# Performance work log

Hardware: AMD Instinct MI355X
Metric: run time of the kernel (lower is better)

Reference implementation:

```python
import jax, jax.numpy as jnp
import numpy as np

N, E, F_IN, H, L, G, NH, HD, C = 50000, 640000, 64, 128, 3, 64, 8, 16, 2


def setup_inputs() -> dict:
    key = jax.random.key(0)
    k = jax.random.split(key, 12)
    s = 0.02
    return {
        "x": jax.random.normal(k[0], (N, F_IN), jnp.float32),
        "edge_index": jax.random.randint(k[1], (2, E), 0, N),
        "batch_idx": jnp.sort(jax.random.randint(k[2], (N,), 0, G)),
        "emb_w": jax.random.normal(k[3], (H, F_IN), jnp.float32) * s,
        "emb_b": jnp.zeros((H,), jnp.float32),
        "gcn_w": jax.random.normal(k[4], (L, H, H), jnp.float32) * s,
        "gcn_b": jnp.zeros((L, H), jnp.float32),
        "lstm_w_ih": jax.random.normal(k[5], (4 * H, H), jnp.float32) * s,
        "lstm_w_hh": jax.random.normal(k[6], (4 * H, H), jnp.float32) * s,
        "lstm_b_ih": jnp.zeros((4 * H,), jnp.float32),
        "lstm_b_hh": jnp.zeros((4 * H,), jnp.float32),
        "attn_in_w": jax.random.normal(k[7], (3 * H, H), jnp.float32) * s,
        "attn_in_b": jnp.zeros((3 * H,), jnp.float32),
        "attn_out_w": jax.random.normal(k[8], (H, H), jnp.float32) * s,
        "attn_out_b": jnp.zeros((H,), jnp.float32),
        "cls_w1": jax.random.normal(k[9], (H // 2, H), jnp.float32) * s,
        "cls_b1": jnp.zeros((H // 2,), jnp.float32),
        "cls_w2": jax.random.normal(k[10], (C, H // 2), jnp.float32) * s,
        "cls_b2": jnp.zeros((C,), jnp.float32),
    }


def reference(x, edge_index, batch_idx, emb_w, emb_b, gcn_w, gcn_b,
              lstm_w_ih, lstm_w_hh, lstm_b_ih, lstm_b_hh,
              attn_in_w, attn_in_b, attn_out_w, attn_out_b,
              cls_w1, cls_b1, cls_w2, cls_b2):
    src, dst = edge_index[0], edge_index[1]
    # GCN symmetric norm with self-loops (PyG gcn_norm): deg includes the self loop
    deg = jax.ops.segment_sum(jnp.ones((E,), x.dtype), dst, num_segments=N) + 1.0
    dis = jax.lax.rsqrt(deg)                      # deg^{-1/2}, deg >= 1
    norm = dis[src] * dis[dst]                    # [E]
    self_norm = dis * dis                         # [N], self-loop weight

    h = x @ emb_w.T + emb_b                       # node embedding [N, H]
    for l in range(L):
        hw = h @ gcn_w[l].T                       # linear transform [N, H]
        agg = jax.ops.segment_sum(hw[src] * norm[:, None], dst, num_segments=N)
        agg = agg + hw * self_norm[:, None]       # self-loop contribution
        h = jax.nn.relu(agg + gcn_b[l])

    # global mean pool per graph
    sums = jax.ops.segment_sum(h, batch_idx, num_segments=G)
    counts = jax.ops.segment_sum(jnp.ones((N,), h.dtype), batch_idx, num_segments=G)
    ge = sums / jnp.maximum(counts, 1.0)[:, None]  # [G, H]

    # LSTM with seq_len=1, h0=c0=0 (W_hh term vanishes); gate order i,f,g,o
    gates = ge @ lstm_w_ih.T + lstm_b_ih + lstm_b_hh
    i, f, g, o = jnp.split(gates, 4, axis=-1)
    c = jax.nn.sigmoid(i) * jnp.tanh(g)
    hs = jax.nn.sigmoid(o) * jnp.tanh(c)           # [G, H]

    # MultiheadAttention, seq_len=1 self-attention
    q, kk, v = jnp.split(hs @ attn_in_w.T + attn_in_b, 3, axis=-1)
    qh = q.reshape(G, NH, HD)
    kh = kk.reshape(G, NH, HD)
    vh = v.reshape(G, NH, HD)
    scores = jnp.einsum('bhd,bhd->bh', qh, kh) / jnp.sqrt(jnp.asarray(HD, hs.dtype))
    attn = jax.nn.softmax(scores[..., None], axis=-1)[..., 0]  # single key -> all ones
    ctx = (attn[..., None] * vh).reshape(G, H)
    fe = ctx @ attn_out_w.T + attn_out_b           # attended_out.mean(dim=1) with S=1

    # classifier (dropout is identity at inference)
    z = jax.nn.relu(fe @ cls_w1.T + cls_b1)
    return z @ cls_w2.T + cls_b2
```

## Files before the change

kernel.cpp:

```cpp
#include <hip/hip_runtime.h>
#include <math.h>

#define N_NODES 50000
#define N_EDGES 640000
#define F_INDIM 64
#define HDIM 128
#define NLAYERS 3
#define NGRAPH 64
#define NCLS 2
#define SCAN_BLOCKS ((N_NODES + 255) / 256)
#define POOL_SPLIT 8
#define NTILES (N_NODES / 16)

typedef __attribute__((ext_vector_type(8))) short bf16x8;
typedef __attribute__((ext_vector_type(4))) float f32x4;

__device__ __forceinline__ float bf_lo(unsigned v) { return __uint_as_float(v << 16); }
__device__ __forceinline__ float bf_hi(unsigned v) { return __uint_as_float(v & 0xffff0000u); }
__device__ __forceinline__ unsigned short f2bf(float f) {
    unsigned b = __float_as_uint(f);
    return (unsigned short)((b + 0x7fffu + ((b >> 16) & 1u)) >> 16);
}


__global__ __launch_bounds__(256) void k_init(int* cnt, float* pool, float* counts) {
    int i = blockIdx.x * 256 + threadIdx.x;
    if (i < N_NODES) cnt[i] = 0;
    if (i < NGRAPH * HDIM) pool[i] = 0.f;
    if (i < NGRAPH) counts[i] = 0.f;
}

__global__ __launch_bounds__(256) void k_rank(const int* __restrict__ dst,
                                              int* __restrict__ cnt,
                                              int* __restrict__ rank) {
    int e = blockIdx.x * 256 + threadIdx.x;
    if (e < N_EDGES) rank[e] = atomicAdd(&cnt[dst[e]], 1);
}

__global__ __launch_bounds__(256) void k_scan1(const int* __restrict__ hist,
                                               int* __restrict__ row_start,
                                               int* __restrict__ partials,
                                               float* __restrict__ dis) {
    __shared__ int buf[256];
    int i = blockIdx.x * 256 + threadIdx.x;
    int v = (i < N_NODES) ? hist[i] : 0;
    if (i < N_NODES) dis[i] = rsqrtf((float)v + 1.0f);
    buf[threadIdx.x] = v;
    __syncthreads();
#pragma unroll
    for (int off = 1; off < 256; off <<= 1) {
        int t = (threadIdx.x >= off) ? buf[threadIdx.x - off] : 0;
        __syncthreads();
        buf[threadIdx.x] += t;
        __syncthreads();
    }
    if (i < N_NODES) row_start[i] = buf[threadIdx.x] - v;
    if (threadIdx.x == 255) partials[blockIdx.x] = buf[255];
}

__global__ __launch_bounds__(256) void k_scan2(int* __restrict__ partials) {
    __shared__ int buf[256];
    int v = (threadIdx.x < SCAN_BLOCKS) ? partials[threadIdx.x] : 0;
    buf[threadIdx.x] = v;
    __syncthreads();
#pragma unroll
    for (int off = 1; off < 256; off <<= 1) {
        int t = (threadIdx.x >= off) ? buf[threadIdx.x - off] : 0;
        __syncthreads();
        buf[threadIdx.x] += t;
        __syncthreads();
    }
    if (threadIdx.x < SCAN_BLOCKS) partials[threadIdx.x] = buf[threadIdx.x] - v;
}

__global__ __launch_bounds__(256) void k_scan3(int* __restrict__ row_start,
                                               const int* __restrict__ partials) {
    int i = blockIdx.x * 256 + threadIdx.x;
    if (i < N_NODES) row_start[i] += partials[blockIdx.x];
    if (i == 0) row_start[N_NODES] = N_EDGES;
}

__global__ __launch_bounds__(256) void k_place(const int* __restrict__ src,
                                               const int* __restrict__ dst,
                                               const int* __restrict__ rank,
                                               const float* __restrict__ dis,
                                               const int* __restrict__ row_start,
                                               uint2* __restrict__ csr) {
    int e = blockIdx.x * 256 + threadIdx.x;
    if (e >= N_EDGES) return;
    int s = src[e], d = dst[e];
    uint2 rec;
    rec.x = (unsigned)s;
    rec.y = __float_as_uint(dis[s] * dis[d]);
    csr[row_start[d] + rank[e]] = rec;
}

#define CVT_Q1 (N_NODES * F_INDIM / 4)
#define CVT_Q2 (CVT_Q1 + HDIM * F_INDIM / 4)
#define CVT_Q3 (CVT_Q2 + NLAYERS * HDIM * HDIM / 4)

__global__ __launch_bounds__(256) void k_cvt_all(const float* __restrict__ x,
                                                 const float* __restrict__ emb_w,
                                                 const float* __restrict__ gcn_w,
                                                 unsigned short* __restrict__ dst0) {
    int i = blockIdx.x * 256 + threadIdx.x;
    if (i >= CVT_Q3) return;
    const float* s;
    int off;
    if (i < CVT_Q1)      { s = x;     off = i; }
    else if (i < CVT_Q2) { s = emb_w; off = i - CVT_Q1; }
    else                 { s = gcn_w; off = i - CVT_Q2; }
    float4 v = *(const float4*)&s[off * 4];
    unsigned r0 = (unsigned)f2bf(v.x) | ((unsigned)f2bf(v.y) << 16);
    unsigned r1 = (unsigned)f2bf(v.z) | ((unsigned)f2bf(v.w) << 16);
    *(uint2*)&dst0[i * 4] = make_uint2(r0, r1);
}


template<int K>
__global__ __launch_bounds__(256) void k_mm(const unsigned short* __restrict__ A,
                                            const unsigned short* __restrict__ W,
                                            const float* __restrict__ bias,
                                            unsigned short* __restrict__ C) {
    constexpr int KS = K / 32;
    int lane = threadIdx.x & 63;
    int lg = lane >> 4, lr = lane & 15;
    int cb = (threadIdx.x >> 6) * 32;
    int tile0 = blockIdx.x * 4;

    bf16x8 wf[2][KS];
#pragma unroll
    for (int ct = 0; ct < 2; ++ct)
#pragma unroll
        for (int ks = 0; ks < KS; ++ks)
            wf[ct][ks] = *(const bf16x8*)&W[(size_t)(cb + ct * 16 + lr) * K + ks * 32 + lg * 8];

    float b0 = bias ? bias[cb + lr] : 0.f;
    float b1 = bias ? bias[cb + 16 + lr] : 0.f;

    int ntile = NTILES - tile0; if (ntile > 4) ntile = 4;
    for (int t = 0; t < ntile; ++t) {
        int rb = (tile0 + t) * 16;
        f32x4 acc0 = {0.f, 0.f, 0.f, 0.f}, acc1 = {0.f, 0.f, 0.f, 0.f};
#pragma unroll
        for (int ks = 0; ks < KS; ++ks) {
            bf16x8 af = *(const bf16x8*)&A[(size_t)(rb + lr) * K + ks * 32 + lg * 8];
            acc0 = __builtin_amdgcn_mfma_f32_16x16x32_bf16(af, wf[0][ks], acc0, 0, 0, 0);
            acc1 = __builtin_amdgcn_mfma_f32_16x16x32_bf16(af, wf[1][ks], acc1, 0, 0, 0);
        }
        int row = rb + lg * 4;
#pragma unroll
        for (int j = 0; j < 4; ++j) {
            C[(size_t)(row + j) * HDIM + cb + lr]      = f2bf(acc0[j] + b0);
            C[(size_t)(row + j) * HDIM + cb + 16 + lr] = f2bf(acc1[j] + b1);
        }
    }
}


__global__ __launch_bounds__(256) void k_gather(const unsigned short* __restrict__ hw,
                                                const int* __restrict__ row_start,
                                                const uint2* __restrict__ csr,
                                                const float* __restrict__ dis,
                                                const float* __restrict__ bias,
                                                unsigned short* __restrict__ hout) {
    int n = blockIdx.x * 4 + (threadIdx.x >> 6);
    int lane = threadIdx.x & 63;
    int half = lane >> 5;
    int cl = lane & 31;
    int beg = row_start[n], end = row_start[n + 1];
    float a0 = 0.f, a1 = 0.f, a2 = 0.f, a3 = 0.f;
    for (int e = beg; e < end; e += 16) {
        unsigned sidx[8]; float w[8]; uint2 v[8];
#pragma unroll
        for (int u = 0; u < 8; ++u) {
            int me = e + 2 * u + half;
            uint2 rec = csr[min(me, end - 1)];
            sidx[u] = rec.x;
            w[u] = (me < end) ? __uint_as_float(rec.y) : 0.f;
        }
#pragma unroll
        for (int u = 0; u < 8; ++u)
            v[u] = *(const uint2*)&hw[(size_t)sidx[u] * HDIM + cl * 4];
#pragma unroll
        for (int u = 0; u < 8; ++u) {
            a0 += w[u] * bf_lo(v[u].x);
            a1 += w[u] * bf_hi(v[u].x);
            a2 += w[u] * bf_lo(v[u].y);
            a3 += w[u] * bf_hi(v[u].y);
        }
    }
    a0 += __shfl_xor(a0, 32); a1 += __shfl_xor(a1, 32);
    a2 += __shfl_xor(a2, 32); a3 += __shfl_xor(a3, 32);
    if (half == 0) {
        float dn = dis[n], sn = dn * dn;
        uint2 vs = *(const uint2*)&hw[(size_t)n * HDIM + cl * 4];
        a0 += sn * bf_lo(vs.x); a1 += sn * bf_hi(vs.x);
        a2 += sn * bf_lo(vs.y); a3 += sn * bf_hi(vs.y);
        float4 b = *(const float4*)&bias[cl * 4];
        a0 = fmaxf(a0 + b.x, 0.f); a1 = fmaxf(a1 + b.y, 0.f);
        a2 = fmaxf(a2 + b.z, 0.f); a3 = fmaxf(a3 + b.w, 0.f);
        uint2 r;
        r.x = (unsigned)f2bf(a0) | ((unsigned)f2bf(a1) << 16);
        r.y = (unsigned)f2bf(a2) | ((unsigned)f2bf(a3) << 16);
        *(uint2*)&hout[(size_t)n * HDIM + cl * 4] = r;
    }
}


__global__ __launch_bounds__(256) void k_pool(const unsigned short* __restrict__ h,
                                              const int* __restrict__ batch,
                                              float* __restrict__ pool,
                                              float* __restrict__ counts) {
    int g  = blockIdx.x >> 3;
    int sp = blockIdx.x & 7;
    int s, e;
    {
        int lo = 0, hi = N_NODES;
        while (lo < hi) { int mid = (lo + hi) >> 1; if (batch[mid] < g) lo = mid + 1; else hi = mid; }
        s = lo;
        lo = s; hi = N_NODES;
        while (lo < hi) { int mid = (lo + hi) >> 1; if (batch[mid] < g + 1) lo = mid + 1; else hi = mid; }
        e = lo;
    }
    int len = e - s;
    int chunk = (len + POOL_SPLIT - 1) / POOL_SPLIT;
    int ss = s + sp * chunk;
    int ee = min(ss + chunk, e);
    int cp = threadIdx.x & 63;
    int r  = threadIdx.x >> 6;
    float a0 = 0.f, a1 = 0.f;
    for (int n = ss + r; n < ee; n += 4) {
        unsigned v = *(const unsigned*)&h[(size_t)n * HDIM + cp * 2];
        a0 += bf_lo(v);
        a1 += bf_hi(v);
    }
    __shared__ float red0[4][64], red1[4][64];
    red0[r][cp] = a0; red1[r][cp] = a1;
    __syncthreads();
    if (r == 0) {
#pragma unroll
        for (int j = 1; j < 4; ++j) { a0 += red0[j][cp]; a1 += red1[j][cp]; }
        atomicAdd(&pool[g * HDIM + cp * 2], a0);
        atomicAdd(&pool[g * HDIM + cp * 2 + 1], a1);
    }
    if (threadIdx.x == 0 && ee > ss) atomicAdd(&counts[g], (float)(ee - ss));
}


__global__ __launch_bounds__(128) void k_tail(const float* __restrict__ pool,
                                              const float* __restrict__ counts,
                                              const float* __restrict__ w_ih,
                                              const float* __restrict__ b_ih,
                                              const float* __restrict__ b_hh,
                                              const float* __restrict__ attn_in_w,
                                              const float* __restrict__ attn_in_b,
                                              const float* __restrict__ attn_out_w,
                                              const float* __restrict__ attn_out_b,
                                              const float* __restrict__ w1,
                                              const float* __restrict__ b1,
                                              const float* __restrict__ w2,
                                              const float* __restrict__ b2,
                                              float* __restrict__ out) {
    __shared__ float ge[128], hsr[128], vv[128], fe[128], zz[64];
    int g = blockIdx.x, t = threadIdx.x;
    float cnt = fmaxf(counts[g], 1.0f);
    ge[t] = pool[g * HDIM + t] / cnt;
    __syncthreads();
    float gi = 0.f, gg = 0.f, go = 0.f;
    for (int k = 0; k < 128; ++k) {
        float xv = ge[k];
        gi += xv * w_ih[t * HDIM + k];
        gg += xv * w_ih[(256 + t) * HDIM + k];
        go += xv * w_ih[(384 + t) * HDIM + k];
    }
    gi += b_ih[t] + b_hh[t];
    gg += b_ih[256 + t] + b_hh[256 + t];
    go += b_ih[384 + t] + b_hh[384 + t];
    float cc = (1.f / (1.f + expf(-gi))) * tanhf(gg);
    float hv = (1.f / (1.f + expf(-go))) * tanhf(cc);
    hsr[t] = hv;
    __syncthreads();
    float va = attn_in_b[256 + t];
    for (int k = 0; k < 128; ++k) va += hsr[k] * attn_in_w[(256 + t) * HDIM + k];
    vv[t] = va;
    __syncthreads();
    float fv = attn_out_b[t];
    for (int k = 0; k < 128; ++k) fv += vv[k] * attn_out_w[t * HDIM + k];
    fe[t] = fv;
    __syncthreads();
    if (t < 64) {
        float zv = b1[t];
        for (int k = 0; k < 128; ++k) zv += fe[k] * w1[t * HDIM + k];
        zz[t] = fmaxf(zv, 0.f);
    }
    __syncthreads();
    if (t < NCLS) {
        float ov = b2[t];
        for (int k = 0; k < 64; ++k) ov += zz[k] * w2[t * 64 + k];
        out[g * NCLS + t] = ov;
    }
}


extern "C" void kernel_launch(void* const* d_in, const int* in_sizes, int n_in,
                              void* d_out, int out_size, void* d_ws, size_t ws_size,
                              hipStream_t stream) {
    const float* x          = (const float*)d_in[0];
    const int*   edge_index = (const int*)d_in[1];
    const int*   batch      = (const int*)d_in[2];
    const float* emb_w      = (const float*)d_in[3];
    const float* emb_b      = (const float*)d_in[4];
    const float* gcn_w      = (const float*)d_in[5];
    const float* gcn_b      = (const float*)d_in[6];
    const float* w_ih       = (const float*)d_in[7];
    const float* b_ih       = (const float*)d_in[9];
    const float* b_hh       = (const float*)d_in[10];
    const float* attn_in_w  = (const float*)d_in[11];
    const float* attn_in_b  = (const float*)d_in[12];
    const float* attn_out_w = (const float*)d_in[13];
    const float* attn_out_b = (const float*)d_in[14];
    const float* w1         = (const float*)d_in[15];
    const float* b1         = (const float*)d_in[16];
    const float* w2         = (const float*)d_in[17];
    const float* b2         = (const float*)d_in[18];
    float* out = (float*)d_out;

    int*   iws = (int*)d_ws;
    float* fws = (float*)d_ws;
    int*   cnt       = iws;
    float* dis       = fws + N_NODES;
    int*   row_start = iws + 2 * N_NODES;
    int*   rank      = iws + 3 * N_NODES + 4;
    uint2* csr       = (uint2*)(iws + 3 * N_NODES + 4 + N_EDGES);
    unsigned short* bws   = (unsigned short*)(iws + 3 * N_NODES + 4 + N_EDGES + 2 * N_EDGES);
    unsigned short* x_bf  = bws;
    unsigned short* we_bf = x_bf + (size_t)N_NODES * F_INDIM;
    unsigned short* wg_bf = we_bf + HDIM * F_INDIM;
    unsigned short* hA    = wg_bf + NLAYERS * HDIM * HDIM;
    unsigned short* hB    = hA + (size_t)N_NODES * HDIM;
    float* pool     = (float*)(hB + (size_t)N_NODES * HDIM);
    float* counts   = pool + NGRAPH * HDIM;
    int*   partials = (int*)(counts + NGRAPH);

    const int* src = edge_index;
    const int* dst = edge_index + N_EDGES;

    k_init<<<196, 256, 0, stream>>>(cnt, pool, counts);
    k_rank<<<(N_EDGES + 255) / 256, 256, 0, stream>>>(dst, cnt, rank);
    k_scan1<<<SCAN_BLOCKS, 256, 0, stream>>>(cnt, row_start, partials, dis);
    k_scan2<<<1, 256, 0, stream>>>(partials);
    k_scan3<<<SCAN_BLOCKS, 256, 0, stream>>>(row_start, partials);
    k_place<<<(N_EDGES + 255) / 256, 256, 0, stream>>>(src, dst, rank, dis, row_start, csr);

    k_cvt_all<<<(CVT_Q3 + 255) / 256, 256, 0, stream>>>(x, emb_w, gcn_w, x_bf);

    int mm_grid = (NTILES + 3) / 4;
    k_mm<F_INDIM><<<mm_grid, 256, 0, stream>>>(x_bf, we_bf, emb_b, hA);
    for (int l = 0; l < NLAYERS; ++l) {
        k_mm<HDIM><<<mm_grid, 256, 0, stream>>>(hA, wg_bf + l * HDIM * HDIM, nullptr, hB);
        k_gather<<<N_NODES / 4, 256, 0, stream>>>(hB, row_start, csr, dis,
                                                  gcn_b + l * HDIM, hA);
    }
    k_pool<<<NGRAPH * POOL_SPLIT, 256, 0, stream>>>(hA, batch, pool, counts);
    k_tail<<<NGRAPH, 128, 0, stream>>>(pool, counts, w_ih, b_ih, b_hh,
                                       attn_in_w, attn_in_b, attn_out_w, attn_out_b,
                                       w1, b1, w2, b2, out);
}
```

Measured before the change: 263.0 us.

## Store node features in column-blocked layout and split gather across feature slices

```diff
diff --git a/kernel.cpp b/kernel.cpp
--- a/kernel.cpp
+++ b/kernel.cpp
@@ -20,6 +20,10 @@
 __device__ __forceinline__ unsigned short f2bf(float f) {
     unsigned b = __float_as_uint(f);
     return (unsigned short)((b + 0x7fffu + ((b >> 16) & 1u)) >> 16);
+}
+
+__device__ __forceinline__ size_t aidx(int row, int c) {
+    return ((size_t)(c >> 4) * N_NODES + row) * 16 + (c & 15);
 }
 
 
@@ -117,7 +121,7 @@
 }
 
 
-template<int K>
+template<int K, bool BLOCKED_A>
 __global__ __launch_bounds__(256) void k_mm(const unsigned short* __restrict__ A,
                                             const unsigned short* __restrict__ W,
                                             const float* __restrict__ bias,
@@ -144,15 +148,18 @@
         f32x4 acc0 = {0.f, 0.f, 0.f, 0.f}, acc1 = {0.f, 0.f, 0.f, 0.f};
 #pragma unroll
         for (int ks = 0; ks < KS; ++ks) {
-            bf16x8 af = *(const bf16x8*)&A[(size_t)(rb + lr) * K + ks * 32 + lg * 8];
+            int c0 = ks * 32 + lg * 8;
+            bf16x8 af = BLOCKED_A
+                ? *(const bf16x8*)&A[aidx(rb + lr, c0)]
+                : *(const bf16x8*)&A[(size_t)(rb + lr) * K + c0];
             acc0 = __builtin_amdgcn_mfma_f32_16x16x32_bf16(af, wf[0][ks], acc0, 0, 0, 0);
             acc1 = __builtin_amdgcn_mfma_f32_16x16x32_bf16(af, wf[1][ks], acc1, 0, 0, 0);
         }
         int row = rb + lg * 4;
 #pragma unroll
         for (int j = 0; j < 4; ++j) {
-            C[(size_t)(row + j) * HDIM + cb + lr]      = f2bf(acc0[j] + b0);
-            C[(size_t)(row + j) * HDIM + cb + 16 + lr] = f2bf(acc1[j] + b1);
+            C[aidx(row + j, cb + lr)]      = f2bf(acc0[j] + b0);
+            C[aidx(row + j, cb + 16 + lr)] = f2bf(acc1[j] + b1);
         }
     }
 }
@@ -164,46 +171,39 @@
                                                 const float* __restrict__ dis,
                                                 const float* __restrict__ bias,
                                                 unsigned short* __restrict__ hout) {
-    int n = blockIdx.x * 4 + (threadIdx.x >> 6);
+    int s = blockIdx.x & 7;
+    int n = (blockIdx.x >> 3) * 4 + (threadIdx.x >> 6);
     int lane = threadIdx.x & 63;
-    int half = lane >> 5;
-    int cl = lane & 31;
+    int u = lane >> 2;
+    int p = lane & 3;
+    size_t sbase = (size_t)s * N_NODES;
     int beg = row_start[n], end = row_start[n + 1];
     float a0 = 0.f, a1 = 0.f, a2 = 0.f, a3 = 0.f;
     for (int e = beg; e < end; e += 16) {
-        unsigned sidx[8]; float w[8]; uint2 v[8];
-#pragma unroll
-        for (int u = 0; u < 8; ++u) {
-            int me = e + 2 * u + half;
-            uint2 rec = csr[min(me, end - 1)];
-            sidx[u] = rec.x;
-            w[u] = (me < end) ? __uint_as_float(rec.y) : 0.f;
-        }
-#pragma unroll
-        for (int u = 0; u < 8; ++u)
-            v[u] = *(const uint2*)&hw[(size_t)sidx[u] * HDIM + cl * 4];
-#pragma unroll
-        for (int u = 0; u < 8; ++u) {
-            a0 += w[u] * bf_lo(v[u].x);
-            a1 += w[u] * bf_hi(v[u].x);
-            a2 += w[u] * bf_lo(v[u].y);
-            a3 += w[u] * bf_hi(v[u].y);
-        }
-    }
-    a0 += __shfl_xor(a0, 32); a1 += __shfl_xor(a1, 32);
-    a2 += __shfl_xor(a2, 32); a3 += __shfl_xor(a3, 32);
-    if (half == 0) {
+        int me = e + u;
+        uint2 rec = csr[min(me, end - 1)];
+        float w = (me < end) ? __uint_as_float(rec.y) : 0.f;
+        uint2 v = *(const uint2*)&hw[(sbase + rec.x) * 16 + p * 4];
+        a0 += w * bf_lo(v.x); a1 += w * bf_hi(v.x);
+        a2 += w * bf_lo(v.y); a3 += w * bf_hi(v.y);
+    }
+#pragma unroll
+    for (int m = 4; m < 64; m <<= 1) {
+        a0 += __shfl_xor(a0, m); a1 += __shfl_xor(a1, m);
+        a2 += __shfl_xor(a2, m); a3 += __shfl_xor(a3, m);
+    }
+    if (u == 0) {
         float dn = dis[n], sn = dn * dn;
-        uint2 vs = *(const uint2*)&hw[(size_t)n * HDIM + cl * 4];
+        uint2 vs = *(const uint2*)&hw[(sbase + n) * 16 + p * 4];
         a0 += sn * bf_lo(vs.x); a1 += sn * bf_hi(vs.x);
         a2 += sn * bf_lo(vs.y); a3 += sn * bf_hi(vs.y);
-        float4 b = *(const float4*)&bias[cl * 4];
+        float4 b = *(const float4*)&bias[s * 16 + p * 4];
         a0 = fmaxf(a0 + b.x, 0.f); a1 = fmaxf(a1 + b.y, 0.f);
         a2 = fmaxf(a2 + b.z, 0.f); a3 = fmaxf(a3 + b.w, 0.f);
         uint2 r;
         r.x = (unsigned)f2bf(a0) | ((unsigned)f2bf(a1) << 16);
         r.y = (unsigned)f2bf(a2) | ((unsigned)f2bf(a3) << 16);
-        *(uint2*)&hout[(size_t)n * HDIM + cl * 4] = r;
+        *(uint2*)&hout[(sbase + n) * 16 + p * 4] = r;
     }
 }
 
@@ -229,9 +229,10 @@
     int ee = min(ss + chunk, e);
     int cp = threadIdx.x & 63;
     int r  = threadIdx.x >> 6;
+    int c0 = cp * 2;
     float a0 = 0.f, a1 = 0.f;
     for (int n = ss + r; n < ee; n += 4) {
-        unsigned v = *(const unsigned*)&h[(size_t)n * HDIM + cp * 2];
+        unsigned v = *(const unsigned*)&h[aidx(n, c0)];
         a0 += bf_lo(v);
         a1 += bf_hi(v);
     }
@@ -241,8 +242,8 @@
     if (r == 0) {
 #pragma unroll
         for (int j = 1; j < 4; ++j) { a0 += red0[j][cp]; a1 += red1[j][cp]; }
-        atomicAdd(&pool[g * HDIM + cp * 2], a0);
-        atomicAdd(&pool[g * HDIM + cp * 2 + 1], a1);
+        atomicAdd(&pool[g * HDIM + c0], a0);
+        atomicAdd(&pool[g * HDIM + c0 + 1], a1);
     }
     if (threadIdx.x == 0 && ee > ss) atomicAdd(&counts[g], (float)(ee - ss));
 }
@@ -356,11 +357,11 @@
     k_cvt_all<<<(CVT_Q3 + 255) / 256, 256, 0, stream>>>(x, emb_w, gcn_w, x_bf);
 
     int mm_grid = (NTILES + 3) / 4;
-    k_mm<F_INDIM><<<mm_grid, 256, 0, stream>>>(x_bf, we_bf, emb_b, hA);
+    k_mm<F_INDIM, false><<<mm_grid, 256, 0, stream>>>(x_bf, we_bf, emb_b, hA);
     for (int l = 0; l < NLAYERS; ++l) {
-        k_mm<HDIM><<<mm_grid, 256, 0, stream>>>(hA, wg_bf + l * HDIM * HDIM, nullptr, hB);
-        k_gather<<<N_NODES / 4, 256, 0, stream>>>(hB, row_start, csr, dis,
-                                                  gcn_b + l * HDIM, hA);
+        k_mm<HDIM, true><<<mm_grid, 256, 0, stream>>>(hA, wg_bf + l * HDIM * HDIM, nullptr, hB);
+        k_gather<<<(N_NODES / 4) * 8, 256, 0, stream>>>(hB, row_start, csr, dis,
+                                                        gcn_b + l * HDIM, hA);
     }
     k_pool<<<NGRAPH * POOL_SPLIT, 256, 0, stream>>>(hA, batch, pool, counts);
     k_tail<<<NGRAPH, 128, 0, stream>>>(pool, counts, w_ih, b_ih, b_hh,
```

Measured after the change: 448.8 us. 1.71x slower.
